# Kernel optimization log

Hardware: AMD Instinct MI355X
Metric: run time of the kernel (lower is better)

The kernel has to match this reference:

```python
import jax, jax.numpy as jnp
import numpy as np

B, S, D = 4, 2048, 1024
H = 16
HD = D // H  # 64


def setup_inputs() -> dict:
    key = jax.random.key(0)
    ks = jax.random.split(key, 5)
    std = 1.0 / np.sqrt(D)
    return {
        "x": jax.random.normal(ks[0], (B, S, D), dtype=jnp.float32),
        "Wq": jax.random.normal(ks[1], (D, D), dtype=jnp.float32) * std,
        "Wk": jax.random.normal(ks[2], (D, D), dtype=jnp.float32) * std,
        "Wv": jax.random.normal(ks[3], (D, D), dtype=jnp.float32) * std,
        "Wo": jax.random.normal(ks[4], (D, D), dtype=jnp.float32) * std,
        "bo": jnp.zeros((D,), dtype=jnp.float32),
    }


def reference(x, Wq, Wk, Wv, Wo, bo):
    b, n, d_in = x.shape
    q = (x @ Wq).reshape(b, n, H, HD).transpose(0, 2, 1, 3)  # [b,h,n,hd]
    k = (x @ Wk).reshape(b, n, H, HD).transpose(0, 2, 1, 3)
    v = (x @ Wv).reshape(b, n, H, HD).transpose(0, 2, 1, 3)
    scores = jnp.einsum("bhqd,bhkd->bhqk", q, k)  # full NxN, as in original
    causal = jnp.tril(jnp.ones((n, n), dtype=bool))  # True = keep
    scores = jnp.where(causal, scores, -jnp.inf)
    attn = jax.nn.softmax(scores / np.sqrt(HD), axis=-1)
    # dropout p=0.0 -> identity
    ctx = jnp.einsum("bhqk,bhkd->bqhd", attn, v).reshape(b, n, H * HD)
    return ctx @ Wo + bo
```

## Files before the change

### kernel.cpp

```cpp
#include <hip/hip_runtime.h>
#include <math.h>

#define BATCH 4
#define SLEN 2048
#define DMODEL 1024
#define NH 16
#define HD 64
#define MROWS (BATCH * SLEN)
#define QK_LD 2048

typedef __attribute__((ext_vector_type(8))) short short8;
typedef __attribute__((ext_vector_type(4))) float floatx4;

#define AS1 __attribute__((address_space(1)))
#define AS3 __attribute__((address_space(3)))

__device__ inline unsigned short f2bf(float f) {
    union { float f; unsigned u; } a; a.f = f;
    unsigned r = a.u + 0x7fff + ((a.u >> 16) & 1);
    return (unsigned short)(r >> 16);
}

__device__ inline unsigned pack_bf(float lo, float hi) {
    union { float f; unsigned u; } a, b; a.f = lo; b.f = hi;
    return __builtin_amdgcn_perm(b.u + 0x8000u, a.u + 0x8000u, 0x07060302u);
}
__device__ inline unsigned pack_tr(float lo, float hi) {
    union { float f; unsigned u; } a, b; a.f = lo; b.f = hi;
    return __builtin_amdgcn_perm(b.u, a.u, 0x07060302u);
}


__global__ __launch_bounds__(256) void cvt_bf16(const float* __restrict__ src,
                                                short* __restrict__ dst) {
    int i = (blockIdx.x * 256 + threadIdx.x) * 4;
    float4 v = *(const float4*)(src + i);
    unsigned short t0 = f2bf(v.x), t1 = f2bf(v.y), t2 = f2bf(v.z), t3 = f2bf(v.w);
    uint2 o;
    o.x = (unsigned)t0 | ((unsigned)t1 << 16);
    o.y = (unsigned)t2 | ((unsigned)t3 << 16);
    *(uint2*)(dst + i) = o;
}

__global__ __launch_bounds__(256) void cvt_wT4(
    const float* __restrict__ Wq, const float* __restrict__ Wk,
    const float* __restrict__ Wv, const float* __restrict__ Wo,
    short* __restrict__ WqkT, short* __restrict__ WvT, short* __restrict__ WoT)
{
    const float* W; short* Wt; float sc = 1.0f;
    int z = blockIdx.z;
    if (z == 0)      { W = Wq; Wt = WqkT; sc = 0.18033688011112042f; }
    else if (z == 1) { W = Wk; Wt = WqkT + (size_t)DMODEL * DMODEL; }
    else if (z == 2) { W = Wv; Wt = WvT; }
    else             { W = Wo; Wt = WoT; }

    __shared__ float t[32][33];
    int bn = blockIdx.x * 32, bk = blockIdx.y * 32;
    int tx = threadIdx.x & 31, r0 = (threadIdx.x >> 5) * 4;
    #pragma unroll
    for (int i = 0; i < 4; i++)
        t[r0 + i][tx] = W[(size_t)(bk + r0 + i) * DMODEL + bn + tx];
    __syncthreads();
    #pragma unroll
    for (int i = 0; i < 4; i++)
        Wt[(size_t)(bn + r0 + i) * DMODEL + bk + tx] = (short)f2bf(t[tx][r0 + i] * sc);
}

#define TM 128
#define TN 128
#define TK 32

template <int OUT_BF16>
__global__ __launch_bounds__(256) void mfma_gemm(
    const short* __restrict__ A,
    const short* __restrict__ Bt,
    const float* __restrict__ bias,
    void* __restrict__ Cout, int M, int N, int K)
{
    __shared__ short As[TM * TK];
    __shared__ short Bs[TN * TK];
    int tid = threadIdx.x;
    int m0 = blockIdx.y * TM, n0 = blockIdx.x * TN;
    int l = tid & 63, w = tid >> 6;
    int wm = (w >> 1) * 64, wn = (w & 1) * 64;
    int lr = l & 15, lk = (l >> 4) * 8;

    floatx4 acc[4][4] = {};

    for (int k0 = 0; k0 < K; k0 += TK) {
        #pragma unroll
        for (int r = 0; r < 2; r++) {
            int c = r * 256 + tid;
            int mm = c >> 2, kk = (c & 3) * 8;
            __builtin_amdgcn_global_load_lds(
                (const AS1 void*)(A + (size_t)(m0 + mm) * K + k0 + kk),
                (AS3 void*)(As + c * 8), 16, 0, 0);
            __builtin_amdgcn_global_load_lds(
                (const AS1 void*)(Bt + (size_t)(n0 + mm) * K + k0 + kk),
                (AS3 void*)(Bs + c * 8), 16, 0, 0);
        }
        __syncthreads();

        short8 af[4], bg[4];
        #pragma unroll
        for (int i = 0; i < 4; i++) {
            af[i] = *(const short8*)(As + (wm + i * 16 + lr) * TK + lk);
            bg[i] = *(const short8*)(Bs + (wn + i * 16 + lr) * TK + lk);
        }
        #pragma unroll
        for (int mi = 0; mi < 4; mi++)
            #pragma unroll
            for (int ni = 0; ni < 4; ni++)
                acc[mi][ni] = __builtin_amdgcn_mfma_f32_16x16x32_bf16(
                    af[mi], bg[ni], acc[mi][ni], 0, 0, 0);
        __syncthreads();
    }

    int rbase = (l >> 4) * 4, cbase = l & 15;
    if (OUT_BF16) {
        short* C = (short*)Cout;
        #pragma unroll
        for (int mi = 0; mi < 4; mi++)
            #pragma unroll
            for (int r = 0; r < 4; r++) {
                int row = m0 + wm + mi * 16 + rbase + r;
                #pragma unroll
                for (int ni = 0; ni < 4; ni++) {
                    int col = n0 + wn + ni * 16 + cbase;
                    C[(size_t)row * N + col] = (short)f2bf(acc[mi][ni][r]);
                }
            }
    } else {
        float* C = (float*)Cout;
        #pragma unroll
        for (int mi = 0; mi < 4; mi++)
            #pragma unroll
            for (int r = 0; r < 4; r++) {
                int row = m0 + wm + mi * 16 + rbase + r;
                #pragma unroll
                for (int ni = 0; ni < 4; ni++) {
                    int col = n0 + wn + ni * 16 + cbase;
                    C[(size_t)row * N + col] = acc[mi][ni][r] + bias[col];
                }
            }
    }
}

#define PSTR 72

__global__ __launch_bounds__(256, 4) void fa_mfma(
    const short* __restrict__ QK, const short* __restrict__ VtT,
    short* __restrict__ ctx)
{
    __shared__ __align__(16) short Ks[2][64][32];
    __shared__ __align__(16) short Vs[2][64][32];
    __shared__ __align__(16) short Ps[4][16][PSTR];

    int tid = threadIdx.x;
    int l = tid & 63, w = tid >> 6;
    int lr = l & 15, lg = l >> 4;
    int bh = blockIdx.x;
    int b = bh >> 4, h = bh & 15;
    int qt = 31 - blockIdx.y;
    int q0 = qt * 64;

    const short* Qbase = QK + (size_t)b * SLEN * QK_LD + h * HD;
    const short* Kbase = Qbase + 1024;
    const short* Vbase = VtT + (size_t)h * HD * MROWS + b * SLEN;

    int xoff = (lg ^ ((lr >> 1) & 3)) * 8;

    short8 ones;
    #pragma unroll
    for (int j = 0; j < 8; j++) ones[j] = (short)0x3F80;

    int qrow = q0 + w * 16 + lr;

    short8 qf[2];
    #pragma unroll
    for (int kk = 0; kk < 2; kk++)
        qf[kk] = *(const short8*)(Qbase + (size_t)qrow * QK_LD + kk * 32 + lg * 8);

    const short* ksrc[2];
    const short* vsrc[2];
    #pragma unroll
    for (int r2 = 0; r2 < 2; r2++) {
        int cc = r2 * 256 + tid;
        int kh = cc >> 8, rr = (cc >> 2) & 63;
        int q = (cc & 3) ^ ((rr >> 1) & 3);
        ksrc[r2] = Kbase + (size_t)rr * QK_LD + kh * 32 + q * 8;
        vsrc[r2] = Vbase + (size_t)rr * MROWS + kh * 32 + q * 8;
    }

    floatx4 O[4] = {};
    floatx4 accL = {};

    for (int kt = 0; kt <= qt; kt++) {
        int k0 = kt * 64;
        __syncthreads();
        #pragma unroll
        for (int r2 = 0; r2 < 2; r2++) {
            int cc = r2 * 256 + tid;
            __builtin_amdgcn_global_load_lds(
                (const AS1 void*)ksrc[r2],
                (AS3 void*)(&Ks[0][0][0] + cc * 8), 16, 0, 0);
            __builtin_amdgcn_global_load_lds(
                (const AS1 void*)vsrc[r2],
                (AS3 void*)(&Vs[0][0][0] + cc * 8), 16, 0, 0);
            ksrc[r2] += (size_t)64 * QK_LD;
            vsrc[r2] += 64;
        }
        __syncthreads();

        floatx4 s4[4] = {};
        #pragma unroll
        for (int kk = 0; kk < 2; kk++)
            #pragma unroll
            for (int t = 0; t < 4; t++) {
                short8 kf = *(const short8*)(&Ks[kk][t * 16 + lr][xoff]);
                s4[t] = __builtin_amdgcn_mfma_f32_16x16x32_bf16(kf, qf[kk], s4[t], 0, 0, 0);
            }

        if (kt == qt) {
            #pragma unroll
            for (int t = 0; t < 4; t++)
                #pragma unroll
                for (int r = 0; r < 4; r++)
                    if (k0 + t * 16 + lg * 4 + r > qrow) s4[t][r] = -INFINITY;
        }

        #pragma unroll
        for (int t = 0; t < 4; t++) {
            float p0 = __builtin_amdgcn_exp2f(s4[t][0]);
            float p1 = __builtin_amdgcn_exp2f(s4[t][1]);
            float p2 = __builtin_amdgcn_exp2f(s4[t][2]);
            float p3 = __builtin_amdgcn_exp2f(s4[t][3]);
            uint2 pk;
            pk.x = pack_tr(p0, p1);
            pk.y = pack_tr(p2, p3);
            *(uint2*)(&Ps[w][lr][t * 16 + lg * 4]) = pk;
        }

        #pragma unroll
        for (int kk = 0; kk < 2; kk++) {
            short8 pf = *(const short8*)(&Ps[w][lr][kk * 32 + lg * 8]);
            accL = __builtin_amdgcn_mfma_f32_16x16x32_bf16(ones, pf, accL, 0, 0, 0);
            #pragma unroll
            for (int dt = 0; dt < 4; dt++) {
                short8 vf = *(const short8*)(&Vs[kk][dt * 16 + lr][xoff]);
                O[dt] = __builtin_amdgcn_mfma_f32_16x16x32_bf16(vf, pf, O[dt], 0, 0, 0);
            }
        }
    }

    float linv = 1.f / accL[0];
    short* crow = ctx + ((size_t)b * SLEN + qrow) * DMODEL + h * HD;
    #pragma unroll
    for (int dt = 0; dt < 4; dt++) {
        uint2 pk;
        pk.x = pack_bf(O[dt][0] * linv, O[dt][1] * linv);
        pk.y = pack_bf(O[dt][2] * linv, O[dt][3] * linv);
        *(uint2*)(crow + dt * 16 + lg * 4) = pk;
    }
}

extern "C" void kernel_launch(void* const* d_in, const int* in_sizes, int n_in,
                              void* d_out, int out_size, void* d_ws, size_t ws_size,
                              hipStream_t stream) {
    const float* x  = (const float*)d_in[0];
    const float* Wq = (const float*)d_in[1];
    const float* Wk = (const float*)d_in[2];
    const float* Wv = (const float*)d_in[3];
    const float* Wo = (const float*)d_in[4];
    const float* bo = (const float*)d_in[5];
    float* out = (float*)d_out;

    const size_t tsz = (size_t)MROWS * DMODEL;
    const size_t wsz = (size_t)DMODEL * DMODEL;

    short* xb    = (short*)d_ws;
    short* WqkT  = xb + tsz;
    short* WvT   = WqkT + 2 * wsz;
    short* WoT   = WvT + wsz;
    short* QKb   = WoT + wsz;
    short* VtT   = QKb + 2 * tsz;
    short* Cb    = VtT + tsz;

    cvt_bf16<<<(int)(tsz / (256 * 4)), 256, 0, stream>>>(x, xb);
    cvt_wT4<<<dim3(32, 32, 4), 256, 0, stream>>>(Wq, Wk, Wv, Wo, WqkT, WvT, WoT);

    mfma_gemm<1><<<dim3(2048 / TN, MROWS / TM), 256, 0, stream>>>(
        xb, WqkT, nullptr, QKb, MROWS, 2048, DMODEL);
    mfma_gemm<1><<<dim3(MROWS / TN, DMODEL / TM), 256, 0, stream>>>(
        WvT, xb, nullptr, VtT, DMODEL, MROWS, DMODEL);

    fa_mfma<<<dim3(BATCH * NH, 32), 256, 0, stream>>>(QKb, VtT, Cb);

    mfma_gemm<0><<<dim3(DMODEL / TN, MROWS / TM), 256, 0, stream>>>(
        Cb, WoT, bo, out, MROWS, DMODEL, DMODEL);
}
```

Measured before the change: 267.0 us.

## Double-buffer LDS tiles in GEMM and flash-attention kernels with async prefetch

Both the MFMA GEMM and the flash-attention kernel now use two LDS buffers. The next K/V (or A/B) tile is issued via global_load_lds before computing on the current one, and explicit vmcnt waits plus raw s_barrier calls replace the double __syncthreads. The goal is to hide global-memory latency behind MFMA work. In exchange it doubles LDS use, which may lower occupancy for fa_mfma, where launch_bounds asks for 4 blocks per CU. It also depends on hand-counted vmcnt values being correct.

```diff
diff --git a/kernel.cpp b/kernel.cpp
--- a/kernel.cpp
+++ b/kernel.cpp
@@ -77,35 +77,61 @@
     const float* __restrict__ bias,
     void* __restrict__ Cout, int M, int N, int K)
 {
-    __shared__ short As[TM * TK];
-    __shared__ short Bs[TN * TK];
+    __shared__ short As[2][TM * TK];
+    __shared__ short Bs[2][TN * TK];
     int tid = threadIdx.x;
     int m0 = blockIdx.y * TM, n0 = blockIdx.x * TN;
     int l = tid & 63, w = tid >> 6;
     int wm = (w >> 1) * 64, wn = (w & 1) * 64;
     int lr = l & 15, lk = (l >> 4) * 8;
 
+    const short* asrc[2];
+    const short* bsrc[2];
+    #pragma unroll
+    for (int r = 0; r < 2; r++) {
+        int c = r * 256 + tid;
+        int mm = c >> 2, kk = (c & 3) * 8;
+        asrc[r] = A  + (size_t)(m0 + mm) * K + kk;
+        bsrc[r] = Bt + (size_t)(n0 + mm) * K + kk;
+    }
+
     floatx4 acc[4][4] = {};
 
-    for (int k0 = 0; k0 < K; k0 += TK) {
-        #pragma unroll
-        for (int r = 0; r < 2; r++) {
-            int c = r * 256 + tid;
-            int mm = c >> 2, kk = (c & 3) * 8;
-            __builtin_amdgcn_global_load_lds(
-                (const AS1 void*)(A + (size_t)(m0 + mm) * K + k0 + kk),
-                (AS3 void*)(As + c * 8), 16, 0, 0);
-            __builtin_amdgcn_global_load_lds(
-                (const AS1 void*)(Bt + (size_t)(n0 + mm) * K + k0 + kk),
-                (AS3 void*)(Bs + c * 8), 16, 0, 0);
-        }
-        __syncthreads();
+    #pragma unroll
+    for (int r = 0; r < 2; r++) {
+        int c = r * 256 + tid;
+        __builtin_amdgcn_global_load_lds((const AS1 void*)asrc[r],
+            (AS3 void*)(&As[0][0] + c * 8), 16, 0, 0);
+        __builtin_amdgcn_global_load_lds((const AS1 void*)bsrc[r],
+            (AS3 void*)(&Bs[0][0] + c * 8), 16, 0, 0);
+        asrc[r] += TK; bsrc[r] += TK;
+    }
+
+    int nk = K / TK;
+    for (int t = 0; t < nk; t++) {
+        int cur = t & 1;
+        if (t + 1 < nk) {
+            #pragma unroll
+            for (int r = 0; r < 2; r++) {
+                int c = r * 256 + tid;
+                __builtin_amdgcn_global_load_lds((const AS1 void*)asrc[r],
+                    (AS3 void*)(&As[cur ^ 1][0] + c * 8), 16, 0, 0);
+                __builtin_amdgcn_global_load_lds((const AS1 void*)bsrc[r],
+                    (AS3 void*)(&Bs[cur ^ 1][0] + c * 8), 16, 0, 0);
+                asrc[r] += TK; bsrc[r] += TK;
+            }
+            asm volatile("s_waitcnt vmcnt(4)" ::: "memory");
+        } else {
+            asm volatile("s_waitcnt vmcnt(0)" ::: "memory");
+        }
+        __builtin_amdgcn_s_barrier();
+        __builtin_amdgcn_sched_barrier(0);
 
         short8 af[4], bg[4];
         #pragma unroll
         for (int i = 0; i < 4; i++) {
-            af[i] = *(const short8*)(As + (wm + i * 16 + lr) * TK + lk);
-            bg[i] = *(const short8*)(Bs + (wn + i * 16 + lr) * TK + lk);
+            af[i] = *(const short8*)(&As[cur][0] + (wm + i * 16 + lr) * TK + lk);
+            bg[i] = *(const short8*)(&Bs[cur][0] + (wn + i * 16 + lr) * TK + lk);
         }
         #pragma unroll
         for (int mi = 0; mi < 4; mi++)
@@ -113,7 +139,9 @@
             for (int ni = 0; ni < 4; ni++)
                 acc[mi][ni] = __builtin_amdgcn_mfma_f32_16x16x32_bf16(
                     af[mi], bg[ni], acc[mi][ni], 0, 0, 0);
-        __syncthreads();
+
+        __builtin_amdgcn_sched_barrier(0);
+        __builtin_amdgcn_s_barrier();
     }
 
     int rbase = (l >> 4) * 4, cbase = l & 15;
@@ -152,8 +180,8 @@
     const short* __restrict__ QK, const short* __restrict__ VtT,
     short* __restrict__ ctx)
 {
-    __shared__ __align__(16) short Ks[2][64][32];
-    __shared__ __align__(16) short Vs[2][64][32];
+    __shared__ __align__(16) short Ks[2][2][64][32];
+    __shared__ __align__(16) short Vs[2][2][64][32];
     __shared__ __align__(16) short Ps[4][16][PSTR];
 
     int tid = threadIdx.x;
@@ -195,29 +223,44 @@
     floatx4 O[4] = {};
     floatx4 accL = {};
 
+    #pragma unroll
+    for (int r2 = 0; r2 < 2; r2++) {
+        int cc = r2 * 256 + tid;
+        __builtin_amdgcn_global_load_lds((const AS1 void*)ksrc[r2],
+            (AS3 void*)(&Ks[0][0][0][0] + cc * 8), 16, 0, 0);
+        __builtin_amdgcn_global_load_lds((const AS1 void*)vsrc[r2],
+            (AS3 void*)(&Vs[0][0][0][0] + cc * 8), 16, 0, 0);
+        ksrc[r2] += (size_t)64 * QK_LD;
+        vsrc[r2] += 64;
+    }
+
     for (int kt = 0; kt <= qt; kt++) {
+        int cur = kt & 1;
         int k0 = kt * 64;
-        __syncthreads();
-        #pragma unroll
-        for (int r2 = 0; r2 < 2; r2++) {
-            int cc = r2 * 256 + tid;
-            __builtin_amdgcn_global_load_lds(
-                (const AS1 void*)ksrc[r2],
-                (AS3 void*)(&Ks[0][0][0] + cc * 8), 16, 0, 0);
-            __builtin_amdgcn_global_load_lds(
-                (const AS1 void*)vsrc[r2],
-                (AS3 void*)(&Vs[0][0][0] + cc * 8), 16, 0, 0);
-            ksrc[r2] += (size_t)64 * QK_LD;
-            vsrc[r2] += 64;
-        }
-        __syncthreads();
+        if (kt < qt) {
+            #pragma unroll
+            for (int r2 = 0; r2 < 2; r2++) {
+                int cc = r2 * 256 + tid;
+                __builtin_amdgcn_global_load_lds((const AS1 void*)ksrc[r2],
+                    (AS3 void*)(&Ks[cur ^ 1][0][0][0] + cc * 8), 16, 0, 0);
+                __builtin_amdgcn_global_load_lds((const AS1 void*)vsrc[r2],
+                    (AS3 void*)(&Vs[cur ^ 1][0][0][0] + cc * 8), 16, 0, 0);
+                ksrc[r2] += (size_t)64 * QK_LD;
+                vsrc[r2] += 64;
+            }
+            asm volatile("s_waitcnt vmcnt(4)" ::: "memory");
+        } else {
+            asm volatile("s_waitcnt vmcnt(0)" ::: "memory");
+        }
+        __builtin_amdgcn_s_barrier();
+        __builtin_amdgcn_sched_barrier(0);
 
         floatx4 s4[4] = {};
         #pragma unroll
         for (int kk = 0; kk < 2; kk++)
             #pragma unroll
             for (int t = 0; t < 4; t++) {
-                short8 kf = *(const short8*)(&Ks[kk][t * 16 + lr][xoff]);
+                short8 kf = *(const short8*)(&Ks[cur][kk][t * 16 + lr][xoff]);
                 s4[t] = __builtin_amdgcn_mfma_f32_16x16x32_bf16(kf, qf[kk], s4[t], 0, 0, 0);
             }
 
@@ -247,10 +290,13 @@
             accL = __builtin_amdgcn_mfma_f32_16x16x32_bf16(ones, pf, accL, 0, 0, 0);
             #pragma unroll
             for (int dt = 0; dt < 4; dt++) {
-                short8 vf = *(const short8*)(&Vs[kk][dt * 16 + lr][xoff]);
+                short8 vf = *(const short8*)(&Vs[cur][kk][dt * 16 + lr][xoff]);
                 O[dt] = __builtin_amdgcn_mfma_f32_16x16x32_bf16(vf, pf, O[dt], 0, 0, 0);
             }
         }
+
+        __builtin_amdgcn_sched_barrier(0);
+        __builtin_amdgcn_s_barrier();
     }
 
     float linv = 1.f / accL[0];
```

Measured after the change: 266.6 us. No clear change (-0.2%).
